# Kernel tuning notes

Measured on AMD Instinct MI355X. Metric: run time of the kernel, lower is better.

The kernel has to match this reference:

```python
import jax, jax.numpy as jnp
import numpy as np

B, N, DIM = 4, 2048, 128
HEADS, HEAD = 8, 128
INNER = HEADS * HEAD  # 1024
EPS = 1e-5


def setup_inputs() -> dict:
    key = jax.random.key(0)
    k0, k1, k2 = jax.random.split(key, 3)
    return {
        "x": jax.random.normal(k0, (B, N, DIM), jnp.float32),
        "ln_gamma": jnp.ones((DIM,), jnp.float32),
        "ln_beta": jnp.zeros((DIM,), jnp.float32),
        "w_qkv": jax.random.normal(k1, (3 * INNER, DIM), jnp.float32) * (DIM ** -0.5),
        "w_out": jax.random.normal(k2, (DIM, INNER), jnp.float32) * (INNER ** -0.5),
        "b_out": jnp.zeros((DIM,), jnp.float32),
    }


def _rope(t):
    """lucidrains-style rotary embedding over full last dim of t: [b,h,n,d]."""
    n, d = t.shape[-2], t.shape[-1]
    inv_freq = 1.0 / (10000.0 ** (jnp.arange(0, d, 2, dtype=jnp.float32) / d))
    freqs = jnp.arange(n, dtype=jnp.float32)[:, None] * inv_freq[None, :]  # [n, d/2]
    freqs = jnp.repeat(freqs, 2, axis=-1)  # interleaved duplicate -> [n, d]
    cos, sin = jnp.cos(freqs), jnp.sin(freqs)
    # rotate_half on interleaved pairs: (x1, x2) -> (-x2, x1)
    x1, x2 = t[..., 0::2], t[..., 1::2]
    rot = jnp.stack((-x2, x1), axis=-1).reshape(t.shape)
    return t * cos + rot * sin


def reference(x, ln_gamma, ln_beta, w_qkv, w_out, b_out):
    # LayerNorm
    mu = x.mean(-1, keepdims=True)
    var = x.var(-1, keepdims=True)
    xn = (x - mu) * jax.lax.rsqrt(var + EPS) * ln_gamma + ln_beta
    # QKV projection (bias-free)
    qkv = jnp.einsum('bnd,ed->bne', xn, w_qkv)  # [B, N, 3*INNER]
    q, k, v = jnp.split(qkv, 3, axis=-1)
    to_heads = lambda t: t.reshape(B, N, HEADS, HEAD).transpose(0, 2, 1, 3)
    q, k, v = to_heads(q), to_heads(k), to_heads(v)  # [B, H, N, HEAD]
    # Partial RoPE: rotate all but the last token; last token stays unrotated
    q = jnp.concatenate([_rope(q[:, :, :-1]), q[:, :, -1:]], axis=2)
    k = jnp.concatenate([_rope(k[:, :, :-1]), k[:, :, -1:]], axis=2)
    scale = HEAD ** -0.5
    dots = jnp.einsum('bhid,bhjd->bhij', q, k) * scale  # [B, H, N, N]
    attn = jax.nn.softmax(dots, axis=-1)
    out = jnp.einsum('bhij,bhjd->bhid', attn, v)
    out = out.transpose(0, 2, 1, 3).reshape(B, N, INNER)
    return out @ w_out.T + b_out
```

## Files before the change

### kernel.cpp

```cpp
#include <hip/hip_runtime.h>
#include <hip/hip_bf16.h>
#include <hip/hip_fp16.h>

#define B_      4
#define N_      2048
#define DIM_    128
#define HEADS_  8
#define HEAD_   128
#define INNER_  1024
#define QKV_    3072
#define EPS_    1e-5f
#define SCALE_  0.08838834764831845f
#define ROPE_C  0.20762050593046015f

typedef __attribute__((ext_vector_type(8))) short short8;
typedef __attribute__((ext_vector_type(4))) short short4v;
typedef __attribute__((ext_vector_type(4))) float f32x4;


__device__ __forceinline__ unsigned short f2bf(float f) {
    unsigned u = __builtin_bit_cast(unsigned, f);
    u = (u + 0x7fffu + ((u >> 16) & 1u)) >> 16;
    return (unsigned short)u;
}
__device__ __forceinline__ float bf2f(unsigned short h) {
    unsigned u = ((unsigned)h) << 16;
    return __builtin_bit_cast(float, u);
}
__device__ __forceinline__ unsigned pk2(float a, float b) {
    return (unsigned)f2bf(a) | ((unsigned)f2bf(b) << 16);
}
__device__ __forceinline__ short4v pack4(const float* e) {
    __hip_bfloat162 h0 = __float22bfloat162_rn(make_float2(e[0], e[1]));
    __hip_bfloat162 h1 = __float22bfloat162_rn(make_float2(e[2], e[3]));
    uint2 u;
    __builtin_memcpy(&u.x, &h0, 4);
    __builtin_memcpy(&u.y, &h1, 4);
    return __builtin_bit_cast(short4v, u);
}

__global__ __launch_bounds__(256) void k_ln(
    const float* __restrict__ x, const float* __restrict__ g,
    const float* __restrict__ be, unsigned short* __restrict__ xnb)
{
    const int w = threadIdx.x >> 6, l = threadIdx.x & 63;
    const int row = blockIdx.x * 4 + w;
    float2 v = *(const float2*)(x + (size_t)row * 128 + l * 2);
    float s = v.x + v.y, s2 = v.x * v.x + v.y * v.y;
#pragma unroll
    for (int off = 1; off < 64; off <<= 1) {
        s  += __shfl_xor(s, off);
        s2 += __shfl_xor(s2, off);
    }
    float mu = s * (1.f / 128.f);
    float var = s2 * (1.f / 128.f) - mu * mu;
    float rs = rsqrtf(var + EPS_);
    float2 gg = *(const float2*)(g + l * 2);
    float2 bb = *(const float2*)(be + l * 2);
    float ox = (v.x - mu) * rs * gg.x + bb.x;
    float oy = (v.y - mu) * rs * gg.y + bb.y;
    *(unsigned*)(xnb + (size_t)row * 128 + l * 2) = pk2(ox, oy);
}

__global__ __launch_bounds__(256) void k_cvt(
    const float* __restrict__ src, unsigned short* __restrict__ dst)
{
    size_t i = ((size_t)blockIdx.x * 256 + threadIdx.x) * 8;
    float4 f0 = *(const float4*)(src + i), f1 = *(const float4*)(src + i + 4);
    uint4 u = { pk2(f0.x, f0.y), pk2(f0.z, f0.w), pk2(f1.x, f1.y), pk2(f1.z, f1.w) };
    *(uint4*)(dst + i) = u;
}

__global__ __launch_bounds__(256) void k_qkvf(
    const unsigned short* __restrict__ xnb, const unsigned short* __restrict__ wb,
    unsigned short* __restrict__ Q, unsigned short* __restrict__ K,
    unsigned short* __restrict__ Vt)
{
    __shared__ unsigned short lA[128 * 136];
    __shared__ unsigned short lB[128 * 136];
    const int t = threadIdx.x;
    const int wv = t >> 6, l = t & 63;
    const int lm = l & 15, quad = l >> 4;
    const int row0 = blockIdx.x * 128;
    const int by   = blockIdx.y;
    const int e0   = by * 128;

#pragma unroll
    for (int i = 0; i < 8; ++i) {
        int c = t + 256 * i;  int r = c >> 4, c8 = c & 15;
        *(uint4*)&lA[r * 136 + c8 * 8] =
            *(const uint4*)(xnb + (size_t)(row0 + r) * 128 + c8 * 8);
        *(uint4*)&lB[r * 136 + c8 * 8] =
            *(const uint4*)(wb + (size_t)(e0 + r) * 128 + c8 * 8);
    }
    __syncthreads();

    short8 af[2][4];
#pragma unroll
    for (int mt = 0; mt < 2; ++mt)
#pragma unroll
        for (int ks = 0; ks < 4; ++ks)
            af[mt][ks] = *(short8*)&lA[(wv * 32 + mt * 16 + lm) * 136 + ks * 32 + quad * 8];

    f32x4 acc[2][8];
#pragma unroll
    for (int mt = 0; mt < 2; ++mt)
#pragma unroll
        for (int ct = 0; ct < 8; ++ct) acc[mt][ct] = (f32x4){0.f, 0.f, 0.f, 0.f};
#pragma unroll
    for (int ks = 0; ks < 4; ++ks) {
#pragma unroll
        for (int ct = 0; ct < 8; ++ct) {
            short8 b = *(short8*)&lB[(ct * 16 + lm) * 136 + ks * 32 + quad * 8];
            acc[0][ct] = __builtin_amdgcn_mfma_f32_16x16x32_bf16(af[0][ks], b, acc[0][ct], 0, 0, 0);
            acc[1][ct] = __builtin_amdgcn_mfma_f32_16x16x32_bf16(af[1][ks], b, acc[1][ct], 0, 0, 0);
        }
    }
    __syncthreads();

    const int b  = row0 >> 11;
    const int n0 = row0 & (N_ - 1);
    const int h  = by & 7;
    const int bh = b * 8 + h;

    if (by < 16) {
#pragma unroll
        for (int mt = 0; mt < 2; ++mt)
#pragma unroll
            for (int ct = 0; ct < 8; ++ct)
#pragma unroll
                for (int r = 0; r < 4; ++r)
                    lA[(wv * 32 + mt * 16 + quad * 4 + r) * 136 + ct * 16 + lm] =
                        f2bf(acc[mt][ct][r]);
        __syncthreads();

        const int r_loc = t >> 1, half = t & 1;
        const int n = n0 + r_loc;
        unsigned short* dst = (by < 8 ? Q : K) +
            ((size_t)bh * N_ + n) * HEAD_ + half * 64;
        const bool dorope = (n != N_ - 1);
#pragma unroll
        for (int j = 0; j < 8; ++j) {
            short8 vv = *(short8*)&lA[r_loc * 136 + half * 64 + j * 8];
            if (dorope) {
                unsigned short* pv = (unsigned short*)&vv;
#pragma unroll
                for (int p = 0; p < 4; ++p) {
                    int i0 = half * 32 + j * 4 + p;
                    float invf = exp2f(-(float)i0 * ROPE_C);
                    float th = (float)n * invf;
                    float cs = __cosf(th), sn = __sinf(th);
                    float e = bf2f(pv[2 * p]), o = bf2f(pv[2 * p + 1]);
                    pv[2 * p]     = f2bf(e * cs - o * sn);
                    pv[2 * p + 1] = f2bf(o * cs + e * sn);
                }
            }
            *(short8*)(dst + j * 8) = vv;
        }
    } else {
#pragma unroll
        for (int mt = 0; mt < 2; ++mt)
#pragma unroll
            for (int ct = 0; ct < 8; ++ct)
#pragma unroll
                for (int r = 0; r < 4; ++r)
                    lA[(ct * 16 + lm) * 136 + wv * 32 + quad * 8 + mt * 4 + r] =
                        f2bf(acc[mt][ct][r]);
        __syncthreads();

        const int d = t >> 1, half = t & 1;
        unsigned short* dst = Vt + ((size_t)bh * HEAD_ + d) * N_ + n0 + half * 64;
#pragma unroll
        for (int j = 0; j < 8; ++j)
            *(short8*)(dst + j * 8) = *(short8*)&lA[d * 136 + half * 64 + j * 8];
    }
}

__global__ __launch_bounds__(256) void k_attn(
    const unsigned short* __restrict__ Q, const unsigned short* __restrict__ K,
    const unsigned short* __restrict__ Vt, unsigned short* __restrict__ Ob)
{
    __shared__ unsigned short lK[64 * 136];
    __shared__ unsigned short lV[128 * 68];

    const int t = threadIdx.x;
    const int w = t >> 6, l = t & 63;
    const int lm = l & 15, quad = l >> 4;
    const int bid = blockIdx.x;
    const int bh = bid & 31;
    const int qt = bid >> 5;
    const int n0 = qt * 128;
    const unsigned short* Qb = Q  + (size_t)bh * N_ * HEAD_;
    const unsigned short* Kb = K  + (size_t)bh * N_ * HEAD_;
    const unsigned short* Vb = Vt + (size_t)bh * N_ * HEAD_;

    short8 aq[2][4];
#pragma unroll
    for (int tt = 0; tt < 2; ++tt) {
        const unsigned short* qp =
            Qb + ((size_t)(n0 + tt * 64 + w * 16 + lm)) * 128 + quad * 8;
#pragma unroll
        for (int ks = 0; ks < 4; ++ks)
            aq[tt][ks] = *(const short8*)(qp + ks * 32);
    }

    f32x4 Oa[2][8];
#pragma unroll
    for (int tt = 0; tt < 2; ++tt)
#pragma unroll
        for (int i = 0; i < 8; ++i) Oa[tt][i] = (f32x4){0.f, 0.f, 0.f, 0.f};
    float ps0 = 0.f, ps1 = 0.f;
    const float C1 = SCALE_ * 1.44269504f;
    const float C0 = -23.08312f;

    short8 kr[4], vr[4];
#pragma unroll
    for (int i = 0; i < 4; ++i) {
        int c = t + 256 * i;
        kr[i] = *(const short8*)(Kb + ((size_t)(c >> 4)) * 128 + (c & 15) * 8);
        vr[i] = *(const short8*)(Vb + (size_t)(c >> 3) * N_ + (c & 7) * 8);
    }

    for (int jt = 0; jt < 32; ++jt) {
        __syncthreads();
#pragma unroll
        for (int i = 0; i < 4; ++i) {
            int c = t + 256 * i;
            *(short8*)&lK[(c >> 4) * 136 + (c & 15) * 8] = kr[i];
            *(short8*)&lV[(c >> 3) * 68  + (c & 7)  * 8] = vr[i];
        }
        __syncthreads();
        if (jt < 31) {
#pragma unroll
            for (int i = 0; i < 4; ++i) {
                int c = t + 256 * i;
                kr[i] = *(const short8*)(Kb + ((size_t)((jt + 1) * 64 + (c >> 4))) * 128 + (c & 15) * 8);
                vr[i] = *(const short8*)(Vb + (size_t)(c >> 3) * N_ + (jt + 1) * 64 + (c & 7) * 8);
            }
        }

        short4v pf0[4], pf1[4];
#pragma unroll
        for (int nb = 0; nb < 4; ++nb) {
            f32x4 st0 = (f32x4){0.f, 0.f, 0.f, 0.f};
            f32x4 st1 = (f32x4){0.f, 0.f, 0.f, 0.f};
#pragma unroll
            for (int ks = 0; ks < 4; ++ks) {
                short8 kf = *(short8*)&lK[(nb * 16 + lm) * 136 + ks * 32 + quad * 8];
                st0 = __builtin_amdgcn_mfma_f32_16x16x32_bf16(kf, aq[0][ks], st0, 0, 0, 0);
                st1 = __builtin_amdgcn_mfma_f32_16x16x32_bf16(kf, aq[1][ks], st1, 0, 0, 0);
            }
            float e0[4], e1[4];
#pragma unroll
            for (int r = 0; r < 4; ++r) {
                e0[r] = exp2f(st0[r] * C1 + C0);
                e1[r] = exp2f(st1[r] * C1 + C0);
                ps0 += e0[r];  ps1 += e1[r];
            }
            pf0[nb] = pack4(e0);
            pf1[nb] = pack4(e1);
        }

#pragma unroll
        for (int c2 = 0; c2 < 2; ++c2) {
            short8 ap0 = __builtin_shufflevector(pf0[2 * c2], pf0[2 * c2 + 1],
                                                 0, 1, 2, 3, 4, 5, 6, 7);
            short8 ap1 = __builtin_shufflevector(pf1[2 * c2], pf1[2 * c2 + 1],
                                                 0, 1, 2, 3, 4, 5, 6, 7);
#pragma unroll
            for (int nb8 = 0; nb8 < 8; ++nb8) {
                short8 bv = *(short8*)&lV[(nb8 * 16 + lm) * 68 + c2 * 32 + quad * 8];
                Oa[0][nb8] = __builtin_amdgcn_mfma_f32_16x16x32_bf16(ap0, bv, Oa[0][nb8], 0, 0, 0);
                Oa[1][nb8] = __builtin_amdgcn_mfma_f32_16x16x32_bf16(ap1, bv, Oa[1][nb8], 0, 0, 0);
            }
        }
    }

    ps0 += __shfl_xor(ps0, 16);  ps0 += __shfl_xor(ps0, 32);
    ps1 += __shfl_xor(ps1, 16);  ps1 += __shfl_xor(ps1, 32);

    const int b = bh >> 3, h = bh & 7;
#pragma unroll
    for (int tt = 0; tt < 2; ++tt)
#pragma unroll
        for (int r = 0; r < 4; ++r) {
            float lsum = __shfl(tt == 0 ? ps0 : ps1, (l & 48) | (quad * 4 + r));
            float il = 1.f / lsum;
            int n = n0 + tt * 64 + w * 16 + quad * 4 + r;
            unsigned short* op = Ob + ((size_t)b * N_ + n) * INNER_ + h * HEAD_ + lm;
#pragma unroll
            for (int nb8 = 0; nb8 < 8; ++nb8)
                op[nb8 * 16] = f2bf(Oa[tt][nb8][r] * il);
        }
}

__global__ __launch_bounds__(256) void k_proj(
    const unsigned short* __restrict__ Ob, const unsigned short* __restrict__ wob,
    const float* __restrict__ bias, float* __restrict__ out)
{
    __shared__ unsigned short lA[64 * 136];
    __shared__ unsigned short lB[64 * 136];
    float* lCf = (float*)lA;
    const int t = threadIdx.x;
    const int wv = t >> 6, l = t & 63;
    const int lm = l & 15, quad = l >> 4;
    const int row0 = blockIdx.x * 64;
    const int e0   = blockIdx.y * 64;

    f32x4 acc[4];
#pragma unroll
    for (int ct = 0; ct < 4; ++ct) acc[ct] = (f32x4){0.f, 0.f, 0.f, 0.f};

    for (int kt = 0; kt < 8; ++kt) {
        __syncthreads();
#pragma unroll
        for (int i = 0; i < 4; ++i) {
            int c = t + 256 * i;  int r = c >> 4, c8 = c & 15;
            *(uint4*)&lA[r * 136 + c8 * 8] =
                *(const uint4*)(Ob + (size_t)(row0 + r) * 1024 + kt * 128 + c8 * 8);
            *(uint4*)&lB[r * 136 + c8 * 8] =
                *(const uint4*)(wob + (size_t)(e0 + r) * 1024 + kt * 128 + c8 * 8);
        }
        __syncthreads();
        short8 a_[4];
#pragma unroll
        for (int ks = 0; ks < 4; ++ks)
            a_[ks] = *(short8*)&lA[(wv * 16 + lm) * 136 + ks * 32 + quad * 8];
#pragma unroll
        for (int ks = 0; ks < 4; ++ks)
#pragma unroll
            for (int ct = 0; ct < 4; ++ct) {
                short8 b = *(short8*)&lB[(ct * 16 + lm) * 136 + ks * 32 + quad * 8];
                acc[ct] = __builtin_amdgcn_mfma_f32_16x16x32_bf16(a_[ks], b, acc[ct], 0, 0, 0);
            }
    }
    __syncthreads();
#pragma unroll
    for (int ct = 0; ct < 4; ++ct)
#pragma unroll
        for (int r = 0; r < 4; ++r)
            lCf[(wv * 16 + quad * 4 + r) * 68 + ct * 16 + lm] = acc[ct][r];
    __syncthreads();
#pragma unroll
    for (int i = 0; i < 4; ++i) {
        int c = t + 256 * i;  int r = c >> 4, c4 = c & 15;
        float4 v = *(float4*)&lCf[r * 68 + c4 * 4];
        float4 b4 = *(const float4*)(bias + e0 + c4 * 4);
        v.x += b4.x; v.y += b4.y; v.z += b4.z; v.w += b4.w;
        *(float4*)(out + (size_t)(row0 + r) * 128 + e0 + c4 * 4) = v;
    }
}

extern "C" void kernel_launch(void* const* d_in, const int* in_sizes, int n_in,
                              void* d_out, int out_size, void* d_ws, size_t ws_size,
                              hipStream_t stream) {
    const float* x      = (const float*)d_in[0];
    const float* gamma  = (const float*)d_in[1];
    const float* beta   = (const float*)d_in[2];
    const float* w_qkv  = (const float*)d_in[3];
    const float* w_out  = (const float*)d_in[4];
    const float* b_out  = (const float*)d_in[5];
    float* out = (float*)d_out;
    char* wsb = (char*)d_ws;
    unsigned short* Q    = (unsigned short*)(wsb);
    unsigned short* K    = (unsigned short*)(wsb + (16ull << 20));
    unsigned short* Vt   = (unsigned short*)(wsb + (32ull << 20));
    unsigned short* Ob   = (unsigned short*)(wsb + (48ull << 20));
    unsigned short* xnb  = (unsigned short*)(wsb + (96ull << 20));
    unsigned short* wqb  = (unsigned short*)(wsb + (98ull << 20));
    unsigned short* wob  = (unsigned short*)(wsb + (99ull << 20));

    k_ln       <<<dim3(2048),    256, 0, stream>>>(x, gamma, beta, xnb);
    k_cvt      <<<dim3(192),     256, 0, stream>>>(w_qkv, wqb);
    k_cvt      <<<dim3(64),      256, 0, stream>>>(w_out, wob);
    k_qkvf     <<<dim3(64, 24),  256, 0, stream>>>(xnb, wqb, Q, K, Vt);
    k_attn     <<<dim3(512),     256, 0, stream>>>(Q, K, Vt, Ob);
    k_proj     <<<dim3(128, 2),  256, 0, stream>>>(Ob, wob, b_out, out);
}
```

Measured before the change: 193.7 us.

## Split attention over two key halves and combine partial outputs

Adds a split-K attention kernel that launches 1024 blocks, each covering half of the key sequence, and writes unnormalized fp32 partial outputs and row sums to workspace. A combine kernel then adds the two halves, normalizes and writes bf16 output. The aim is to double the block count and fill more of the CUs that the previous 512-block launch left underused. In exchange it adds an extra launch and about 64MB of fp32 partial writes and reads. It runs only when the workspace is large enough, otherwise it falls back to the old kernel.

Result: slower. 210.5 us (+8.6%).

```diff
diff --git a/kernel.cpp b/kernel.cpp
--- a/kernel.cpp
+++ b/kernel.cpp
@@ -292,6 +292,159 @@
             for (int nb8 = 0; nb8 < 8; ++nb8)
                 op[nb8 * 16] = f2bf(Oa[tt][nb8][r] * il);
         }
+}
+
+__global__ __launch_bounds__(256) void k_attn2(
+    const unsigned short* __restrict__ Q, const unsigned short* __restrict__ K,
+    const unsigned short* __restrict__ Vt, float* __restrict__ Opart,
+    float* __restrict__ psb)
+{
+    __shared__ unsigned short lK[64 * 136];
+    __shared__ unsigned short lV[128 * 68];
+
+    const int t = threadIdx.x;
+    const int w = t >> 6, l = t & 63;
+    const int lm = l & 15, quad = l >> 4;
+    const int bid = blockIdx.x;
+    const int s   = bid >> 9;
+    const int p   = bid & 511;
+    const int bh  = bid & 31;
+    const int qt  = (bid >> 5) & 15;
+    const int n0  = qt * 128;
+    const int jt0 = s * 16;
+    const unsigned short* Qb = Q  + (size_t)bh * N_ * HEAD_;
+    const unsigned short* Kb = K  + (size_t)bh * N_ * HEAD_;
+    const unsigned short* Vb = Vt + (size_t)bh * N_ * HEAD_;
+
+    short8 aq[2][4];
+#pragma unroll
+    for (int tt = 0; tt < 2; ++tt) {
+        const unsigned short* qp =
+            Qb + ((size_t)(n0 + tt * 64 + w * 16 + lm)) * 128 + quad * 8;
+#pragma unroll
+        for (int ks = 0; ks < 4; ++ks)
+            aq[tt][ks] = *(const short8*)(qp + ks * 32);
+    }
+
+    f32x4 Oa[2][8];
+#pragma unroll
+    for (int tt = 0; tt < 2; ++tt)
+#pragma unroll
+        for (int i = 0; i < 8; ++i) Oa[tt][i] = (f32x4){0.f, 0.f, 0.f, 0.f};
+    float ps0 = 0.f, ps1 = 0.f;
+    const float C1 = SCALE_ * 1.44269504f;
+    const float C0 = -23.08312f;
+
+    short8 kr[4], vr[4];
+#pragma unroll
+    for (int i = 0; i < 4; ++i) {
+        int c = t + 256 * i;
+        kr[i] = *(const short8*)(Kb + ((size_t)(jt0 * 64 + (c >> 4))) * 128 + (c & 15) * 8);
+        vr[i] = *(const short8*)(Vb + (size_t)(c >> 3) * N_ + jt0 * 64 + (c & 7) * 8);
+    }
+
+    for (int jt = 0; jt < 16; ++jt) {
+        __syncthreads();
+#pragma unroll
+        for (int i = 0; i < 4; ++i) {
+            int c = t + 256 * i;
+            *(short8*)&lK[(c >> 4) * 136 + (c & 15) * 8] = kr[i];
+            *(short8*)&lV[(c >> 3) * 68  + (c & 7)  * 8] = vr[i];
+        }
+        __syncthreads();
+        if (jt < 15) {
+#pragma unroll
+            for (int i = 0; i < 4; ++i) {
+                int c = t + 256 * i;
+                kr[i] = *(const short8*)(Kb + ((size_t)((jt0 + jt + 1) * 64 + (c >> 4))) * 128 + (c & 15) * 8);
+                vr[i] = *(const short8*)(Vb + (size_t)(c >> 3) * N_ + (jt0 + jt + 1) * 64 + (c & 7) * 8);
+            }
+        }
+
+        short4v pf0[4], pf1[4];
+#pragma unroll
+        for (int nb = 0; nb < 4; ++nb) {
+            f32x4 st0 = (f32x4){0.f, 0.f, 0.f, 0.f};
+            f32x4 st1 = (f32x4){0.f, 0.f, 0.f, 0.f};
+#pragma unroll
+            for (int ks = 0; ks < 4; ++ks) {
+                short8 kf = *(short8*)&lK[(nb * 16 + lm) * 136 + ks * 32 + quad * 8];
+                st0 = __builtin_amdgcn_mfma_f32_16x16x32_bf16(kf, aq[0][ks], st0, 0, 0, 0);
+                st1 = __builtin_amdgcn_mfma_f32_16x16x32_bf16(kf, aq[1][ks], st1, 0, 0, 0);
+            }
+            float e0[4], e1[4];
+#pragma unroll
+            for (int r = 0; r < 4; ++r) {
+                e0[r] = exp2f(st0[r] * C1 + C0);
+                e1[r] = exp2f(st1[r] * C1 + C0);
+                ps0 += e0[r];  ps1 += e1[r];
+            }
+            pf0[nb] = pack4(e0);
+            pf1[nb] = pack4(e1);
+        }
+
+#pragma unroll
+        for (int c2 = 0; c2 < 2; ++c2) {
+            short8 ap0 = __builtin_shufflevector(pf0[2 * c2], pf0[2 * c2 + 1],
+                                                 0, 1, 2, 3, 4, 5, 6, 7);
+            short8 ap1 = __builtin_shufflevector(pf1[2 * c2], pf1[2 * c2 + 1],
+                                                 0, 1, 2, 3, 4, 5, 6, 7);
+#pragma unroll
+            for (int nb8 = 0; nb8 < 8; ++nb8) {
+                short8 bv = *(short8*)&lV[(nb8 * 16 + lm) * 68 + c2 * 32 + quad * 8];
+                Oa[0][nb8] = __builtin_amdgcn_mfma_f32_16x16x32_bf16(ap0, bv, Oa[0][nb8], 0, 0, 0);
+                Oa[1][nb8] = __builtin_amdgcn_mfma_f32_16x16x32_bf16(ap1, bv, Oa[1][nb8], 0, 0, 0);
+            }
+        }
+    }
+
+    ps0 += __shfl_xor(ps0, 16);  ps0 += __shfl_xor(ps0, 32);
+    ps1 += __shfl_xor(ps1, 16);  ps1 += __shfl_xor(ps1, 32);
+
+    float* Op = Opart + ((size_t)(s * 512 + p)) * 16384;
+    float* pp = psb   + ((size_t)(s * 512 + p)) * 128;
+#pragma unroll
+    for (int tt = 0; tt < 2; ++tt)
+#pragma unroll
+        for (int r = 0; r < 4; ++r) {
+            float lsum = __shfl(tt == 0 ? ps0 : ps1, (l & 48) | (quad * 4 + r));
+            int rowl = tt * 64 + w * 16 + quad * 4 + r;
+            if (lm == 0) pp[rowl] = lsum;
+#pragma unroll
+            for (int nb8 = 0; nb8 < 8; ++nb8)
+                Op[rowl * 128 + nb8 * 16 + lm] = Oa[tt][nb8][r];
+        }
+}
+
+__global__ __launch_bounds__(256) void k_comb(
+    const float* __restrict__ Opart, const float* __restrict__ psb,
+    unsigned short* __restrict__ Ob)
+{
+    __shared__ float inv[128];
+    const int p = blockIdx.x;
+    const int t = threadIdx.x;
+    const int bh = p & 31, qt = p >> 5;
+    if (t < 128) {
+        float d = psb[(size_t)p * 128 + t] + psb[(size_t)(512 + p) * 128 + t];
+        inv[t] = 1.f / d;
+    }
+    __syncthreads();
+    const float* O0 = Opart + (size_t)p * 16384;
+    const float* O1 = Opart + (size_t)(512 + p) * 16384;
+    const int b = bh >> 3, h = bh & 7;
+#pragma unroll
+    for (int i = 0; i < 16; ++i) {
+        int flat = i * 256 + t;
+        int row = flat >> 5, dq = (flat & 31) * 4;
+        float4 a = *(const float4*)(O0 + row * 128 + dq);
+        float4 c = *(const float4*)(O1 + row * 128 + dq);
+        float iv = inv[row];
+        float e[4] = { (a.x + c.x) * iv, (a.y + c.y) * iv,
+                       (a.z + c.z) * iv, (a.w + c.w) * iv };
+        short4v o = pack4(e);
+        int n = qt * 128 + row;
+        *(short4v*)(Ob + ((size_t)b * N_ + n) * INNER_ + h * HEAD_ + dq) = o;
+    }
 }
 
 __global__ __launch_bounds__(256) void k_proj(
@@ -374,6 +527,14 @@
     k_cvt      <<<dim3(192),     256, 0, stream>>>(w_qkv, wqb);
     k_cvt      <<<dim3(64),      256, 0, stream>>>(w_out, wob);
     k_qkvf     <<<dim3(64, 24),  256, 0, stream>>>(xnb, wqb, Q, K, Vt);
-    k_attn     <<<dim3(512),     256, 0, stream>>>(Q, K, Vt, Ob);
+
+    if (ws_size >= (165ull << 20)) {
+        float* Opart = (float*)(wsb + (100ull << 20));
+        float* psb   = (float*)(wsb + (164ull << 20));
+        k_attn2 <<<dim3(1024), 256, 0, stream>>>(Q, K, Vt, Opart, psb);
+        k_comb  <<<dim3(512),  256, 0, stream>>>(Opart, psb, Ob);
+    } else {
+        k_attn  <<<dim3(512),  256, 0, stream>>>(Q, K, Vt, Ob);
+    }
     k_proj     <<<dim3(128, 2),  256, 0, stream>>>(Ob, wob, b_out, out);
 }
```
